# Kernel optimization log

Measured on AMD Instinct MI355X. Metric: run time of the kernel, lower is better.

## Reference

```python
import jax, jax.numpy as jnp
import numpy as np

B, L, D, K, NRBF = 2, 2048, 128, 3, 16
NUM_ATOMS = 118


def setup_inputs() -> dict:
    key = jax.random.key(0)
    ks = jax.random.split(key, 20)
    s = 0.05
    inp = {
        "coords": jax.random.normal(ks[0], (B, L, 3), dtype=jnp.float32) * 3.0,
        "Z": jax.random.randint(ks[1], (B, L), 0, NUM_ATOMS),
        # CoordEncoder params
        "atom_emb": jax.random.normal(ks[2], (NUM_ATOMS, D), dtype=jnp.float32) * s,
        "gamma": jnp.asarray(10.0, dtype=jnp.float32),
        "rbf_centers": jnp.linspace(0.0, 5.0, NRBF, dtype=jnp.float32),
        "rbf_w": jax.random.normal(ks[3], (NRBF, D), dtype=jnp.float32) * s,
        "rbf_b": jnp.zeros((D,), dtype=jnp.float32),
        "out_w": jax.random.normal(ks[4], (2 * D, D), dtype=jnp.float32) * s,
        "out_b": jnp.zeros((D,), dtype=jnp.float32),
        # MP_Layer params, stacked over K layers
        "self_w": jax.random.normal(ks[5], (K, D, D), dtype=jnp.float32) * s,
        "self_b": jnp.zeros((K, D), dtype=jnp.float32),
        "msg_w": jax.random.normal(ks[6], (K, D, D), dtype=jnp.float32) * s,
        "msg_b": jnp.zeros((K, D), dtype=jnp.float32),
        "upd_w": jax.random.normal(ks[7], (K, 2 * D, D), dtype=jnp.float32) * s,
        "upd_b": jnp.zeros((K, D), dtype=jnp.float32),
    }
    return inp


def _pairwise_dist(coords):
    # coords: [B,L,3] -> dist: [B,L,L]; safe sqrt so diagonal has zero grad
    diff = coords[:, :, None, :] - coords[:, None, :, :]
    sq = jnp.sum(diff * diff, axis=-1)
    return jnp.where(sq > 0, jnp.sqrt(jnp.where(sq > 0, sq, 1.0)), 0.0)


def reference(coords, Z, atom_emb, gamma, rbf_centers, rbf_w, rbf_b,
              out_w, out_b, self_w, self_b, msg_w, msg_b, upd_w, upd_b):
    # --- CoordEncoder ---
    h_atom = atom_emb[Z]                                   # [B,L,D]
    dist = _pairwise_dist(coords)                          # [B,L,L]
    rbf = jnp.exp(-gamma * (dist[..., None] - rbf_centers) ** 2)  # [B,L,L,R]
    rbf_local = rbf.mean(axis=2)                           # [B,L,R]
    h_geo = rbf_local @ rbf_w + rbf_b                      # [B,L,D]
    h = jnp.concatenate([h_atom, h_geo], axis=-1) @ out_w + out_b  # [B,L,D]
    # --- MP layers (mask is None; W = exp(-dist) is the same every layer) ---
    W = jnp.exp(-dist)                                     # [B,L,L]
    for k in range(K):
        msg = jnp.einsum("bij,bjd->bid", W, h @ msg_w[k] + msg_b[k])
        h = jnp.concatenate([h @ self_w[k] + self_b[k], msg], axis=-1) @ upd_w[k] + upd_b[k]
    return h
```

## Files before the change

### kernel.cpp

```cpp
#include <hip/hip_runtime.h>
#include <hip/hip_bf16.h>

typedef unsigned short u16;
typedef __bf16 bf16x8 __attribute__((ext_vector_type(8)));
typedef float f32x4 __attribute__((ext_vector_type(4)));
typedef u16 u16x4 __attribute__((ext_vector_type(4)));

#define B_ 2
#define L_ 2048
#define D_ 128
#define KLAY 3
#define NR 16
#define NATOM 118
#define DD (D_ * D_)
#define XTN (L_ * D_)

static __device__ __forceinline__ u16 f2bf(float f) {
    union { float f; unsigned u; } v; v.f = f;
    unsigned r = v.u + 0x7FFFu + ((v.u >> 16) & 1u);
    return (u16)(r >> 16);
}
static __device__ __forceinline__ bf16x8 ld_bf8(const u16* p) {
    return *(const bf16x8*)p;
}

__global__ __launch_bounds__(256) void prep_kernel(
    const float* atom_emb, const float* out_w, const float* self_w,
    const float* msg_w, const float* upd_w,
    u16* atom16, u16* outwT, u16* selfT, u16* msgT, u16* updT) {
    const int T0 = NATOM * D_;
    const int T1 = D_ * 2 * D_;
    const int T2 = KLAY * DD;
    const int T3 = KLAY * DD;
    const int T4 = KLAY * 2 * DD;
    int total = T0 + T1 + T2 + T3 + T4;
    for (int t = blockIdx.x * blockDim.x + threadIdx.x; t < total;
         t += gridDim.x * blockDim.x) {
        int u = t;
        if (u < T0) { atom16[u] = f2bf(atom_emb[u]); continue; }
        u -= T0;
        if (u < T1) {
            int n = u / (2 * D_), k = u % (2 * D_);
            outwT[u] = f2bf(out_w[k * D_ + n]);
            continue;
        }
        u -= T1;
        if (u < T2) {
            int kk = u / DD, v = u % DD;
            int n = v / D_, k = v % D_;
            selfT[u] = f2bf(self_w[kk * DD + k * D_ + n]);
            continue;
        }
        u -= T2;
        if (u < T3) {
            int kk = u / DD, v = u % DD;
            int n = v / D_, k = v % D_;
            msgT[u] = f2bf(msg_w[kk * DD + k * D_ + n]);
            continue;
        }
        u -= T3;
        {
            int kk = u / (2 * DD), v = u % (2 * DD);
            int n = v / (2 * D_), k = v % (2 * D_);
            updT[u] = f2bf(upd_w[kk * 2 * DD + k * D_ + n]);
        }
    }
}

__global__ __launch_bounds__(256) void rbf_kernel(
    const float* coords, const float* gamma_p, const float* centers,
    float* rbf_loc) {
    int w = threadIdx.x >> 6, lane = threadIdx.x & 63;
    int bi = blockIdx.x * 4 + w;
    int b = bi >> 11;
    float gamma = gamma_p[0];
    float dl = centers[1] - centers[0];
    float c4[4];
#pragma unroll
    for (int g = 0; g < 4; g++) c4[g] = centers[4 * g];
    float two_gdl = 2.f * gamma * dl;
    float cx = coords[bi * 3 + 0];
    float cy = coords[bi * 3 + 1];
    float cz = coords[bi * 3 + 2];
    const float* cb = coords + (size_t)b * L_ * 3;
    float acc[4][4];
#pragma unroll
    for (int g = 0; g < 4; g++)
#pragma unroll
        for (int m = 0; m < 4; m++) acc[g][m] = 0.f;
    for (int it = 0; it < L_ / 64; it++) {
        int j = lane + 64 * it;
        float dx = cx - cb[j * 3 + 0];
        float dy = cy - cb[j * 3 + 1];
        float dz = cz - cb[j * 3 + 2];
        float sq = dx * dx + dy * dy + dz * dz;
        float d = sq > 0.f ? sqrtf(sq) : 0.f;
#pragma unroll
        for (int g = 0; g < 4; g++) {
            float x = d - c4[g];
            float base = __expf(-gamma * x * x);
            float u = __expf(fminf(two_gdl * x, 29.f));
            float p = base;
            acc[g][0] += p;
            p *= u; acc[g][1] += p;
            p *= u; acc[g][2] += p;
            p *= u; acc[g][3] += p;
        }
    }
#pragma unroll
    for (int off = 32; off > 0; off >>= 1)
#pragma unroll
        for (int g = 0; g < 4; g++)
#pragma unroll
            for (int m = 0; m < 4; m++) acc[g][m] += __shfl_xor(acc[g][m], off);
    if (lane == 0) {
#pragma unroll
        for (int m = 0; m < 4; m++) {
            float Km = __expf(-gamma * (m * dl) * (m * dl)) * (1.0f / L_);
#pragma unroll
            for (int g = 0; g < 4; g++)
                rbf_loc[(size_t)bi * NR + 4 * g + m] = acc[g][m] * Km;
        }
    }
}

__global__ __launch_bounds__(256) void enc_sx_kernel(
    const int* Z, const float* rbf_w, const float* rbf_b, const float* out_b,
    const float* rbf_loc, const u16* atom16, const u16* outwT,
    const u16* selfT0, const u16* msgT0, const float* self_b0, const float* msg_b0,
    u16* S16, u16* XT16) {
    int gi0 = blockIdx.x * 16;
    int b = gi0 >> 11;
    int il0 = gi0 & (L_ - 1);
    int tid = threadIdx.x;
    __shared__ __align__(16) u16 hgeo[16][136];
    __shared__ __align__(16) u16 h_lds[16][136];
    for (int e = tid; e < 16 * D_; e += 256) {
        int row = e >> 7, d = e & 127;
        int gi = gi0 + row;
        float s = rbf_b[d];
#pragma unroll
        for (int r = 0; r < NR; r++)
            s += rbf_loc[(size_t)gi * NR + r] * rbf_w[r * D_ + d];
        hgeo[row][d] = f2bf(s);
    }
    __syncthreads();
    int w = tid >> 6, lane = tid & 63;
    int rowf = lane & 15, kg = lane >> 4;
    f32x4 z = {0.f, 0.f, 0.f, 0.f};
    f32x4 acc[2] = {z, z};
    int za = Z[gi0 + rowf];
    for (int ks = 0; ks < 8; ks++) {
        int k0 = ks * 32 + kg * 8;
        bf16x8 a;
        if (k0 < 128) a = ld_bf8(atom16 + za * D_ + k0);
        else a = ld_bf8(&hgeo[rowf][k0 - 128]);
#pragma unroll
        for (int q = 0; q < 2; q++) {
            int cl = (w * 2 + q) * 16 + rowf;
            bf16x8 bb = ld_bf8(outwT + cl * (2 * D_) + k0);
            acc[q] = __builtin_amdgcn_mfma_f32_16x16x32_bf16(a, bb, acc[q], 0, 0, 0);
        }
    }
#pragma unroll
    for (int q = 0; q < 2; q++) {
        int cl = (w * 2 + q) * 16 + rowf;
        float bias = out_b[cl];
#pragma unroll
        for (int r = 0; r < 4; r++) h_lds[kg * 4 + r][cl] = f2bf(acc[q][r] + bias);
    }
    __syncthreads();
    f32x4 acc3[4] = {z, z, z, z};
    for (int ks = 0; ks < 4; ks++) {
        int k0 = ks * 32 + kg * 8;
        bf16x8 a = ld_bf8(&h_lds[rowf][k0]);
#pragma unroll
        for (int q = 0; q < 4; q++) {
            int nb = w * 4 + q;
            const u16* wp = (nb < 8) ? (selfT0 + (nb * 16 + rowf) * D_ + k0)
                                     : (msgT0 + ((nb - 8) * 16 + rowf) * D_ + k0);
            acc3[q] = __builtin_amdgcn_mfma_f32_16x16x32_bf16(a, ld_bf8(wp), acc3[q], 0, 0, 0);
        }
    }
#pragma unroll
    for (int q = 0; q < 4; q++) {
        int nb = w * 4 + q;
        if (nb < 8) {
            int cl = nb * 16 + rowf;
            float bias = self_b0[cl];
#pragma unroll
            for (int r = 0; r < 4; r++)
                S16[(size_t)(gi0 + kg * 4 + r) * D_ + cl] = f2bf(acc3[q][r] + bias);
        } else {
            int cl = (nb - 8) * 16 + rowf;
            float bias = msg_b0[cl];
            u16x4 pk;
#pragma unroll
            for (int r = 0; r < 4; r++) pk[r] = f2bf(acc3[q][r] + bias);
            int jj = il0 + kg * 4;
            *(u16x4*)(XT16 + (size_t)b * XTN + (jj >> 5) * (32 * D_) + cl * 32 + (jj & 31)) = pk;
        }
    }
}

__global__ __launch_bounds__(512, 2) void mp_fused_kernel(
    const float* coords, const u16* XT_in, const u16* S_in,
    const u16* updT_k, const float* upd_b_k,
    const u16* selfTn, const u16* msgTn, const float* self_bn, const float* msg_bn,
    u16* S_out, u16* XT_out, float* out_f32, int last) {
    int gi0 = blockIdx.x * 16;
    int b = gi0 >> 11;
    int il0 = gi0 & (L_ - 1);
    int tid = threadIdx.x;
    int w = tid >> 6, lane = tid & 63;
    int rowf = lane & 15, kg = lane >> 4;

    __shared__ __align__(16) float red[4][16][128];
    __shared__ __align__(16) float cj[L_ * 3];
    u16* msg_lds = (u16*)&red[0][0][0];
    u16* h_lds = (u16*)&red[1][0][0];

    {
        const float4* src = (const float4*)(coords + (size_t)b * L_ * 3);
        float4* dst = (float4*)cj;
#pragma unroll
        for (int i = 0; i < 3; i++) dst[tid + i * 512] = src[tid + i * 512];
    }
    __syncthreads();

    float rx = cj[(il0 + rowf) * 3 + 0];
    float ry = cj[(il0 + rowf) * 3 + 1];
    float rz = cj[(il0 + rowf) * 3 + 2];

    f32x4 z = {0.f, 0.f, 0.f, 0.f};
    f32x4 acc[8] = {z, z, z, z, z, z, z, z};
    const u16* xbase = XT_in + (size_t)b * XTN + (w * 8) * (32 * D_) + rowf * 32 + kg * 8;
#pragma unroll
    for (int s = 0; s < 8; s++) {
        int j0 = w * 256 + s * 32 + kg * 8;
        const float* jc = &cj[j0 * 3];
        union { bf16x8 v; __bf16 e[8]; } wf;
#pragma unroll
        for (int e = 0; e < 8; e++) {
            float dx = rx - jc[e * 3 + 0];
            float dy = ry - jc[e * 3 + 1];
            float dz = rz - jc[e * 3 + 2];
            float sq = dx * dx + dy * dy + dz * dz;
            float d = sq > 0.f ? sqrtf(sq) : 0.f;
            wf.e[e] = (__bf16)__expf(-d);
        }
#pragma unroll
        for (int n = 0; n < 8; n++) {
            bf16x8 bb = ld_bf8(xbase + s * (32 * D_) + n * 512);
            acc[n] = __builtin_amdgcn_mfma_f32_16x16x32_bf16(wf.v, bb, acc[n], 0, 0, 0);
        }
    }
    auto stash = [&](int slot) {
#pragma unroll
        for (int n = 0; n < 8; n++)
#pragma unroll
            for (int r = 0; r < 4; r++) {
                int row = kg * 4 + r, col = n * 16 + rowf;
                red[slot][row][(col + 4 * row) & 127] = acc[n][r];
            }
    };
    auto grab = [&](int slot) {
#pragma unroll
        for (int n = 0; n < 8; n++)
#pragma unroll
            for (int r = 0; r < 4; r++) {
                int row = kg * 4 + r, col = n * 16 + rowf;
                acc[n][r] += red[slot][row][(col + 4 * row) & 127];
            }
    };
    if (w >= 4) stash(w - 4);
    __syncthreads();
    if (w < 4) grab(w);
    if (w == 2 || w == 3) stash(w);
    __syncthreads();
    if (w < 2) grab(w + 2);
    if (w == 1) stash(3);
    __syncthreads();
    if (w == 0) {
        grab(3);
#pragma unroll
        for (int n = 0; n < 8; n++)
#pragma unroll
            for (int r = 0; r < 4; r++)
                msg_lds[(kg * 4 + r) * 136 + n * 16 + rowf] = f2bf(acc[n][r]);
    }
    __syncthreads();
    f32x4 acc2 = z;
    int cl = w * 16 + rowf;
#pragma unroll
    for (int ks = 0; ks < 8; ks++) {
        int k0 = ks * 32 + kg * 8;
        bf16x8 av = (ks < 4) ? ld_bf8(S_in + (size_t)(gi0 + rowf) * D_ + k0)
                             : ld_bf8(msg_lds + rowf * 136 + (k0 - 128));
        acc2 = __builtin_amdgcn_mfma_f32_16x16x32_bf16(
            av, ld_bf8(updT_k + cl * 2 * D_ + k0), acc2, 0, 0, 0);
    }
    float bias = upd_b_k[cl];
    if (last) {
#pragma unroll
        for (int r = 0; r < 4; r++)
            out_f32[(size_t)(gi0 + kg * 4 + r) * D_ + cl] = acc2[r] + bias;
        return;
    }
#pragma unroll
    for (int r = 0; r < 4; r++)
        h_lds[(kg * 4 + r) * 136 + cl] = f2bf(acc2[r] + bias);
    __syncthreads();
    f32x4 a30 = z, a31 = z;
#pragma unroll
    for (int ks = 0; ks < 4; ks++) {
        int k0 = ks * 32 + kg * 8;
        bf16x8 av = ld_bf8(h_lds + rowf * 136 + k0);
        a30 = __builtin_amdgcn_mfma_f32_16x16x32_bf16(
            av, ld_bf8(selfTn + cl * D_ + k0), a30, 0, 0, 0);
        a31 = __builtin_amdgcn_mfma_f32_16x16x32_bf16(
            av, ld_bf8(msgTn + cl * D_ + k0), a31, 0, 0, 0);
    }
    float bs = self_bn[cl], bm = msg_bn[cl];
#pragma unroll
    for (int r = 0; r < 4; r++)
        S_out[(size_t)(gi0 + kg * 4 + r) * D_ + cl] = f2bf(a30[r] + bs);
    u16x4 pk;
#pragma unroll
    for (int r = 0; r < 4; r++) pk[r] = f2bf(a31[r] + bm);
    int jj = il0 + kg * 4;
    *(u16x4*)(XT_out + (size_t)b * XTN + (jj >> 5) * (32 * D_) + cl * 32 + (jj & 31)) = pk;
}

extern "C" void kernel_launch(void* const* d_in, const int* in_sizes, int n_in,
                              void* d_out, int out_size, void* d_ws, size_t ws_size,
                              hipStream_t stream) {
    const float* coords = (const float*)d_in[0];
    const int* Z = (const int*)d_in[1];
    const float* atom_emb = (const float*)d_in[2];
    const float* gamma = (const float*)d_in[3];
    const float* centers = (const float*)d_in[4];
    const float* rbf_w = (const float*)d_in[5];
    const float* rbf_b = (const float*)d_in[6];
    const float* out_w = (const float*)d_in[7];
    const float* out_b = (const float*)d_in[8];
    const float* self_w = (const float*)d_in[9];
    const float* self_b = (const float*)d_in[10];
    const float* msg_w = (const float*)d_in[11];
    const float* msg_b = (const float*)d_in[12];
    const float* upd_w = (const float*)d_in[13];
    const float* upd_b = (const float*)d_in[14];
    float* out = (float*)d_out;

    char* ws = (char*)d_ws;
    u16* S_a = (u16*)(ws + 0);
    u16* S_b = (u16*)(ws + 1048576);
    u16* XT_a = (u16*)(ws + 2097152);
    u16* XT_b = (u16*)(ws + 3145728);
    float* rbfl = (float*)(ws + 4194304);
    u16* atom16 = (u16*)(ws + 4456448);
    u16* outwT = (u16*)(ws + 4489216);
    u16* selfT = (u16*)(ws + 4554752);
    u16* msgT = (u16*)(ws + 4653056);
    u16* updT = (u16*)(ws + 4751360);

    prep_kernel<<<64, 256, 0, stream>>>(atom_emb, out_w, self_w, msg_w, upd_w,
                                        atom16, outwT, selfT, msgT, updT);
    rbf_kernel<<<(B_ * L_) / 4, 256, 0, stream>>>(coords, gamma, centers, rbfl);
    enc_sx_kernel<<<(B_ * L_) / 16, 256, 0, stream>>>(
        Z, rbf_w, rbf_b, out_b, rbfl, atom16, outwT,
        selfT, msgT, self_b, msg_b, S_a, XT_a);
    mp_fused_kernel<<<256, 512, 0, stream>>>(
        coords, XT_a, S_a, updT + 0 * 2 * DD, upd_b + 0 * D_,
        selfT + 1 * DD, msgT + 1 * DD, self_b + 1 * D_, msg_b + 1 * D_,
        S_b, XT_b, out, 0);
    mp_fused_kernel<<<256, 512, 0, stream>>>(
        coords, XT_b, S_b, updT + 1 * 2 * DD, upd_b + 1 * D_,
        selfT + 2 * DD, msgT + 2 * DD, self_b + 2 * D_, msg_b + 2 * D_,
        S_a, XT_a, out, 0);
    mp_fused_kernel<<<256, 512, 0, stream>>>(
        coords, XT_a, S_a, updT + 2 * 2 * DD, upd_b + 2 * D_,
        selfT, msgT, self_b, msg_b, S_b, XT_b, out, 1);
}
```

Measured before the change: 108.1 us.

## Fuse all stages into one cooperative persistent kernel with grid syncs

Replaces the six separate launches (weight prep, RBF, encoder, three MP layers) with one cooperative kernel of 256 blocks that uses grid.sync between phases. The RBF reduction and encoder now run per 16-row tile out of LDS-resident coordinates, and the self-projection S is kept in LDS instead of being round-tripped through global memory. The goal is to remove launch gaps and intermediate global traffic. In exchange it adds grid-wide barriers, and it relies on all 256 blocks of 512 threads being co-resident for the cooperative launch.

```diff
diff --git a/kernel.cpp b/kernel.cpp
--- a/kernel.cpp
+++ b/kernel.cpp
@@ -1,5 +1,8 @@
 #include <hip/hip_runtime.h>
 #include <hip/hip_bf16.h>
+#include <hip/hip_cooperative_groups.h>
+
+namespace cg = cooperative_groups;
 
 typedef unsigned short u16;
 typedef __bf16 bf16x8 __attribute__((ext_vector_type(8)));
@@ -24,312 +27,292 @@
     return *(const bf16x8*)p;
 }
 
-__global__ __launch_bounds__(256) void prep_kernel(
-    const float* atom_emb, const float* out_w, const float* self_w,
-    const float* msg_w, const float* upd_w,
+__global__ __launch_bounds__(512, 2) void uber_kernel(
+    const float* coords, const int* Z, const float* atom_emb,
+    const float* gamma_p, const float* centers, const float* rbf_w,
+    const float* rbf_b, const float* out_w, const float* out_b,
+    const float* self_w, const float* self_b, const float* msg_w,
+    const float* msg_b, const float* upd_w, const float* upd_b,
+    float* out_f32, u16* XT_a, u16* XT_b,
     u16* atom16, u16* outwT, u16* selfT, u16* msgT, u16* updT) {
-    const int T0 = NATOM * D_;
-    const int T1 = D_ * 2 * D_;
-    const int T2 = KLAY * DD;
-    const int T3 = KLAY * DD;
-    const int T4 = KLAY * 2 * DD;
-    int total = T0 + T1 + T2 + T3 + T4;
-    for (int t = blockIdx.x * blockDim.x + threadIdx.x; t < total;
-         t += gridDim.x * blockDim.x) {
-        int u = t;
-        if (u < T0) { atom16[u] = f2bf(atom_emb[u]); continue; }
-        u -= T0;
-        if (u < T1) {
-            int n = u / (2 * D_), k = u % (2 * D_);
-            outwT[u] = f2bf(out_w[k * D_ + n]);
-            continue;
-        }
-        u -= T1;
-        if (u < T2) {
-            int kk = u / DD, v = u % DD;
-            int n = v / D_, k = v % D_;
-            selfT[u] = f2bf(self_w[kk * DD + k * D_ + n]);
-            continue;
-        }
-        u -= T2;
-        if (u < T3) {
-            int kk = u / DD, v = u % DD;
-            int n = v / D_, k = v % D_;
-            msgT[u] = f2bf(msg_w[kk * DD + k * D_ + n]);
-            continue;
-        }
-        u -= T3;
-        {
-            int kk = u / (2 * DD), v = u % (2 * DD);
-            int n = v / (2 * D_), k = v % (2 * D_);
-            updT[u] = f2bf(upd_w[kk * 2 * DD + k * D_ + n]);
-        }
-    }
-}
-
-__global__ __launch_bounds__(256) void rbf_kernel(
-    const float* coords, const float* gamma_p, const float* centers,
-    float* rbf_loc) {
-    int w = threadIdx.x >> 6, lane = threadIdx.x & 63;
-    int bi = blockIdx.x * 4 + w;
-    int b = bi >> 11;
-    float gamma = gamma_p[0];
-    float dl = centers[1] - centers[0];
-    float c4[4];
-#pragma unroll
-    for (int g = 0; g < 4; g++) c4[g] = centers[4 * g];
-    float two_gdl = 2.f * gamma * dl;
-    float cx = coords[bi * 3 + 0];
-    float cy = coords[bi * 3 + 1];
-    float cz = coords[bi * 3 + 2];
-    const float* cb = coords + (size_t)b * L_ * 3;
-    float acc[4][4];
-#pragma unroll
-    for (int g = 0; g < 4; g++)
-#pragma unroll
-        for (int m = 0; m < 4; m++) acc[g][m] = 0.f;
-    for (int it = 0; it < L_ / 64; it++) {
-        int j = lane + 64 * it;
-        float dx = cx - cb[j * 3 + 0];
-        float dy = cy - cb[j * 3 + 1];
-        float dz = cz - cb[j * 3 + 2];
-        float sq = dx * dx + dy * dy + dz * dz;
-        float d = sq > 0.f ? sqrtf(sq) : 0.f;
-#pragma unroll
-        for (int g = 0; g < 4; g++) {
-            float x = d - c4[g];
-            float base = __expf(-gamma * x * x);
-            float u = __expf(fminf(two_gdl * x, 29.f));
-            float p = base;
-            acc[g][0] += p;
-            p *= u; acc[g][1] += p;
-            p *= u; acc[g][2] += p;
-            p *= u; acc[g][3] += p;
-        }
-    }
-#pragma unroll
-    for (int off = 32; off > 0; off >>= 1)
-#pragma unroll
-        for (int g = 0; g < 4; g++)
-#pragma unroll
-            for (int m = 0; m < 4; m++) acc[g][m] += __shfl_xor(acc[g][m], off);
-    if (lane == 0) {
-#pragma unroll
-        for (int m = 0; m < 4; m++) {
-            float Km = __expf(-gamma * (m * dl) * (m * dl)) * (1.0f / L_);
-#pragma unroll
-            for (int g = 0; g < 4; g++)
-                rbf_loc[(size_t)bi * NR + 4 * g + m] = acc[g][m] * Km;
-        }
-    }
-}
-
-__global__ __launch_bounds__(256) void enc_sx_kernel(
-    const int* Z, const float* rbf_w, const float* rbf_b, const float* out_b,
-    const float* rbf_loc, const u16* atom16, const u16* outwT,
-    const u16* selfT0, const u16* msgT0, const float* self_b0, const float* msg_b0,
-    u16* S16, u16* XT16) {
-    int gi0 = blockIdx.x * 16;
-    int b = gi0 >> 11;
-    int il0 = gi0 & (L_ - 1);
-    int tid = threadIdx.x;
-    __shared__ __align__(16) u16 hgeo[16][136];
-    __shared__ __align__(16) u16 h_lds[16][136];
-    for (int e = tid; e < 16 * D_; e += 256) {
-        int row = e >> 7, d = e & 127;
-        int gi = gi0 + row;
-        float s = rbf_b[d];
-#pragma unroll
-        for (int r = 0; r < NR; r++)
-            s += rbf_loc[(size_t)gi * NR + r] * rbf_w[r * D_ + d];
-        hgeo[row][d] = f2bf(s);
-    }
-    __syncthreads();
-    int w = tid >> 6, lane = tid & 63;
-    int rowf = lane & 15, kg = lane >> 4;
-    f32x4 z = {0.f, 0.f, 0.f, 0.f};
-    f32x4 acc[2] = {z, z};
-    int za = Z[gi0 + rowf];
-    for (int ks = 0; ks < 8; ks++) {
-        int k0 = ks * 32 + kg * 8;
-        bf16x8 a;
-        if (k0 < 128) a = ld_bf8(atom16 + za * D_ + k0);
-        else a = ld_bf8(&hgeo[rowf][k0 - 128]);
-#pragma unroll
-        for (int q = 0; q < 2; q++) {
-            int cl = (w * 2 + q) * 16 + rowf;
-            bf16x8 bb = ld_bf8(outwT + cl * (2 * D_) + k0);
-            acc[q] = __builtin_amdgcn_mfma_f32_16x16x32_bf16(a, bb, acc[q], 0, 0, 0);
-        }
-    }
-#pragma unroll
-    for (int q = 0; q < 2; q++) {
-        int cl = (w * 2 + q) * 16 + rowf;
-        float bias = out_b[cl];
-#pragma unroll
-        for (int r = 0; r < 4; r++) h_lds[kg * 4 + r][cl] = f2bf(acc[q][r] + bias);
-    }
-    __syncthreads();
-    f32x4 acc3[4] = {z, z, z, z};
-    for (int ks = 0; ks < 4; ks++) {
-        int k0 = ks * 32 + kg * 8;
-        bf16x8 a = ld_bf8(&h_lds[rowf][k0]);
-#pragma unroll
-        for (int q = 0; q < 4; q++) {
-            int nb = w * 4 + q;
-            const u16* wp = (nb < 8) ? (selfT0 + (nb * 16 + rowf) * D_ + k0)
-                                     : (msgT0 + ((nb - 8) * 16 + rowf) * D_ + k0);
-            acc3[q] = __builtin_amdgcn_mfma_f32_16x16x32_bf16(a, ld_bf8(wp), acc3[q], 0, 0, 0);
-        }
-    }
-#pragma unroll
-    for (int q = 0; q < 4; q++) {
-        int nb = w * 4 + q;
-        if (nb < 8) {
-            int cl = nb * 16 + rowf;
-            float bias = self_b0[cl];
-#pragma unroll
-            for (int r = 0; r < 4; r++)
-                S16[(size_t)(gi0 + kg * 4 + r) * D_ + cl] = f2bf(acc3[q][r] + bias);
-        } else {
-            int cl = (nb - 8) * 16 + rowf;
-            float bias = msg_b0[cl];
-            u16x4 pk;
-#pragma unroll
-            for (int r = 0; r < 4; r++) pk[r] = f2bf(acc3[q][r] + bias);
-            int jj = il0 + kg * 4;
-            *(u16x4*)(XT16 + (size_t)b * XTN + (jj >> 5) * (32 * D_) + cl * 32 + (jj & 31)) = pk;
-        }
-    }
-}
-
-__global__ __launch_bounds__(512, 2) void mp_fused_kernel(
-    const float* coords, const u16* XT_in, const u16* S_in,
-    const u16* updT_k, const float* upd_b_k,
-    const u16* selfTn, const u16* msgTn, const float* self_bn, const float* msg_bn,
-    u16* S_out, u16* XT_out, float* out_f32, int last) {
-    int gi0 = blockIdx.x * 16;
-    int b = gi0 >> 11;
-    int il0 = gi0 & (L_ - 1);
-    int tid = threadIdx.x;
-    int w = tid >> 6, lane = tid & 63;
-    int rowf = lane & 15, kg = lane >> 4;
-
+    cg::grid_group grid = cg::this_grid();
+    const int rt = blockIdx.x;
+    const int gi0 = rt * 16;
+    const int b = gi0 >> 11;
+    const int il0 = gi0 & (L_ - 1);
+    const int tid = threadIdx.x;
+    const int w = tid >> 6, lane = tid & 63;
+    const int rowf = lane & 15, kg = lane >> 4;
+
+    __shared__ __align__(16) float cj[L_ * 3];
     __shared__ __align__(16) float red[4][16][128];
-    __shared__ __align__(16) float cj[L_ * 3];
+    __shared__ float rbf_lds[16][NR];
+    __shared__ __align__(16) u16 s_lds[16][136];
     u16* msg_lds = (u16*)&red[0][0][0];
     u16* h_lds = (u16*)&red[1][0][0];
+    u16* hgeo = (u16*)&red[2][0][0];
+
+    for (int i = tid; i < 1536; i += 512)
+        ((float4*)cj)[i] = ((const float4*)(coords + (size_t)b * L_ * 3))[i];
 
     {
-        const float4* src = (const float4*)(coords + (size_t)b * L_ * 3);
-        float4* dst = (float4*)cj;
-#pragma unroll
-        for (int i = 0; i < 3; i++) dst[tid + i * 512] = src[tid + i * 512];
+        const int T0 = NATOM * D_;
+        const int T1 = D_ * 2 * D_;
+        const int T2 = KLAY * DD;
+        const int T3 = KLAY * DD;
+        const int T4 = KLAY * 2 * DD;
+        const int total = T0 + T1 + T2 + T3 + T4;
+        for (int t = rt * 512 + tid; t < total; t += 256 * 512) {
+            int u = t;
+            if (u < T0) { atom16[u] = f2bf(atom_emb[u]); continue; }
+            u -= T0;
+            if (u < T1) {
+                int n = u / (2 * D_), k = u % (2 * D_);
+                outwT[u] = f2bf(out_w[k * D_ + n]);
+                continue;
+            }
+            u -= T1;
+            if (u < T2) {
+                int kk = u / DD, v = u % DD;
+                int n = v / D_, k = v % D_;
+                selfT[u] = f2bf(self_w[kk * DD + k * D_ + n]);
+                continue;
+            }
+            u -= T2;
+            if (u < T3) {
+                int kk = u / DD, v = u % DD;
+                int n = v / D_, k = v % D_;
+                msgT[u] = f2bf(msg_w[kk * DD + k * D_ + n]);
+                continue;
+            }
+            u -= T3;
+            {
+                int kk = u / (2 * DD), v = u % (2 * DD);
+                int n = v / (2 * D_), k = v % (2 * D_);
+                updT[u] = f2bf(upd_w[kk * 2 * DD + k * D_ + n]);
+            }
+        }
     }
     __syncthreads();
+
+    {
+        int row = tid >> 5, s = tid & 31;
+        float gamma = gamma_p[0];
+        float dl = centers[1] - centers[0];
+        float c4[4];
+#pragma unroll
+        for (int g = 0; g < 4; g++) c4[g] = centers[4 * g];
+        float two_gdl = 2.f * gamma * dl;
+        float cx = cj[(il0 + row) * 3 + 0];
+        float cy = cj[(il0 + row) * 3 + 1];
+        float cz = cj[(il0 + row) * 3 + 2];
+        float acc[4][4];
+#pragma unroll
+        for (int g = 0; g < 4; g++)
+#pragma unroll
+            for (int m = 0; m < 4; m++) acc[g][m] = 0.f;
+        for (int it = 0; it < 64; it++) {
+            int j = s + 32 * it;
+            float dx = cx - cj[j * 3 + 0];
+            float dy = cy - cj[j * 3 + 1];
+            float dz = cz - cj[j * 3 + 2];
+            float sq = dx * dx + dy * dy + dz * dz;
+            float d = sq > 0.f ? sqrtf(sq) : 0.f;
+#pragma unroll
+            for (int g = 0; g < 4; g++) {
+                float x = d - c4[g];
+                float base = __expf(-gamma * x * x);
+                float u = __expf(fminf(two_gdl * x, 29.f));
+                float p = base;
+                acc[g][0] += p;
+                p *= u; acc[g][1] += p;
+                p *= u; acc[g][2] += p;
+                p *= u; acc[g][3] += p;
+            }
+        }
+#pragma unroll
+        for (int off = 16; off > 0; off >>= 1)
+#pragma unroll
+            for (int g = 0; g < 4; g++)
+#pragma unroll
+                for (int m = 0; m < 4; m++) acc[g][m] += __shfl_xor(acc[g][m], off);
+        if (s == 0) {
+#pragma unroll
+            for (int m = 0; m < 4; m++) {
+                float Km = __expf(-gamma * (m * dl) * (m * dl)) * (1.0f / L_);
+#pragma unroll
+                for (int g = 0; g < 4; g++)
+                    rbf_lds[row][4 * g + m] = acc[g][m] * Km;
+            }
+        }
+    }
+    grid.sync();
+
+    f32x4 z = {0.f, 0.f, 0.f, 0.f};
+
+    for (int e = tid; e < 16 * D_; e += 512) {
+        int row = e >> 7, d = e & 127;
+        float s = rbf_b[d];
+#pragma unroll
+        for (int r = 0; r < NR; r++) s += rbf_lds[row][r] * rbf_w[r * D_ + d];
+        hgeo[row * 136 + d] = f2bf(s);
+    }
+    __syncthreads();
+
+    {
+        f32x4 a1 = z;
+        int za = Z[gi0 + rowf];
+        int cl = w * 16 + rowf;
+#pragma unroll
+        for (int ks = 0; ks < 8; ks++) {
+            int k0 = ks * 32 + kg * 8;
+            bf16x8 av = (k0 < 128) ? ld_bf8(atom16 + za * D_ + k0)
+                                   : ld_bf8(hgeo + rowf * 136 + (k0 - 128));
+            a1 = __builtin_amdgcn_mfma_f32_16x16x32_bf16(
+                av, ld_bf8(outwT + cl * 2 * D_ + k0), a1, 0, 0, 0);
+        }
+        float bias = out_b[cl];
+#pragma unroll
+        for (int r = 0; r < 4; r++) h_lds[(kg * 4 + r) * 136 + cl] = f2bf(a1[r] + bias);
+    }
+    __syncthreads();
+
+    {
+        int cl = w * 16 + rowf;
+        f32x4 a30 = z, a31 = z;
+#pragma unroll
+        for (int ks = 0; ks < 4; ks++) {
+            int k0 = ks * 32 + kg * 8;
+            bf16x8 av = ld_bf8(h_lds + rowf * 136 + k0);
+            a30 = __builtin_amdgcn_mfma_f32_16x16x32_bf16(
+                av, ld_bf8(selfT + cl * D_ + k0), a30, 0, 0, 0);
+            a31 = __builtin_amdgcn_mfma_f32_16x16x32_bf16(
+                av, ld_bf8(msgT + cl * D_ + k0), a31, 0, 0, 0);
+        }
+        float bs = self_b[cl], bm = msg_b[cl];
+#pragma unroll
+        for (int r = 0; r < 4; r++) s_lds[kg * 4 + r][cl] = f2bf(a30[r] + bs);
+        u16x4 pk;
+#pragma unroll
+        for (int r = 0; r < 4; r++) pk[r] = f2bf(a31[r] + bm);
+        int jj = il0 + kg * 4;
+        *(u16x4*)(XT_a + (size_t)b * XTN + (jj >> 5) * (32 * D_) + cl * 32 + (jj & 31)) = pk;
+    }
+    grid.sync();
 
     float rx = cj[(il0 + rowf) * 3 + 0];
     float ry = cj[(il0 + rowf) * 3 + 1];
     float rz = cj[(il0 + rowf) * 3 + 2];
-
-    f32x4 z = {0.f, 0.f, 0.f, 0.f};
-    f32x4 acc[8] = {z, z, z, z, z, z, z, z};
-    const u16* xbase = XT_in + (size_t)b * XTN + (w * 8) * (32 * D_) + rowf * 32 + kg * 8;
-#pragma unroll
-    for (int s = 0; s < 8; s++) {
-        int j0 = w * 256 + s * 32 + kg * 8;
-        const float* jc = &cj[j0 * 3];
-        union { bf16x8 v; __bf16 e[8]; } wf;
-#pragma unroll
-        for (int e = 0; e < 8; e++) {
-            float dx = rx - jc[e * 3 + 0];
-            float dy = ry - jc[e * 3 + 1];
-            float dz = rz - jc[e * 3 + 2];
-            float sq = dx * dx + dy * dy + dz * dz;
-            float d = sq > 0.f ? sqrtf(sq) : 0.f;
-            wf.e[e] = (__bf16)__expf(-d);
-        }
-#pragma unroll
-        for (int n = 0; n < 8; n++) {
-            bf16x8 bb = ld_bf8(xbase + s * (32 * D_) + n * 512);
-            acc[n] = __builtin_amdgcn_mfma_f32_16x16x32_bf16(wf.v, bb, acc[n], 0, 0, 0);
-        }
-    }
-    auto stash = [&](int slot) {
-#pragma unroll
-        for (int n = 0; n < 8; n++)
-#pragma unroll
-            for (int r = 0; r < 4; r++) {
-                int row = kg * 4 + r, col = n * 16 + rowf;
-                red[slot][row][(col + 4 * row) & 127] = acc[n][r];
-            }
-    };
-    auto grab = [&](int slot) {
-#pragma unroll
-        for (int n = 0; n < 8; n++)
-#pragma unroll
-            for (int r = 0; r < 4; r++) {
-                int row = kg * 4 + r, col = n * 16 + rowf;
-                acc[n][r] += red[slot][row][(col + 4 * row) & 127];
-            }
-    };
-    if (w >= 4) stash(w - 4);
-    __syncthreads();
-    if (w < 4) grab(w);
-    if (w == 2 || w == 3) stash(w);
-    __syncthreads();
-    if (w < 2) grab(w + 2);
-    if (w == 1) stash(3);
-    __syncthreads();
-    if (w == 0) {
-        grab(3);
-#pragma unroll
-        for (int n = 0; n < 8; n++)
+    const u16* XTin = XT_a;
+    u16* XTout = XT_b;
+
+    for (int k = 0; k < KLAY; k++) {
+        f32x4 acc[8] = {z, z, z, z, z, z, z, z};
+        const u16* xbase = XTin + (size_t)b * XTN + (w * 8) * (32 * D_) + rowf * 32 + kg * 8;
+#pragma unroll
+        for (int s = 0; s < 8; s++) {
+            int j0 = w * 256 + s * 32 + kg * 8;
+            union { bf16x8 v; __bf16 e[8]; } wf;
+#pragma unroll
+            for (int e = 0; e < 8; e++) {
+                int jl = j0 + e;
+                float dx = rx - cj[jl * 3 + 0];
+                float dy = ry - cj[jl * 3 + 1];
+                float dz = rz - cj[jl * 3 + 2];
+                float sq = dx * dx + dy * dy + dz * dz;
+                float d = sq > 0.f ? sqrtf(sq) : 0.f;
+                wf.e[e] = (__bf16)__expf(-d);
+            }
+#pragma unroll
+            for (int n = 0; n < 8; n++) {
+                bf16x8 bb = ld_bf8(xbase + s * (32 * D_) + n * 512);
+                acc[n] = __builtin_amdgcn_mfma_f32_16x16x32_bf16(wf.v, bb, acc[n], 0, 0, 0);
+            }
+        }
+        auto stash = [&](int slot) {
+#pragma unroll
+            for (int n = 0; n < 8; n++)
+#pragma unroll
+                for (int r = 0; r < 4; r++) {
+                    int row = kg * 4 + r, col = n * 16 + rowf;
+                    red[slot][row][(col + 4 * row) & 127] = acc[n][r];
+                }
+        };
+        auto grab = [&](int slot) {
+#pragma unroll
+            for (int n = 0; n < 8; n++)
+#pragma unroll
+                for (int r = 0; r < 4; r++) {
+                    int row = kg * 4 + r, col = n * 16 + rowf;
+                    acc[n][r] += red[slot][row][(col + 4 * row) & 127];
+                }
+        };
+        __syncthreads();
+        if (w >= 4) stash(w - 4);
+        __syncthreads();
+        if (w < 4) grab(w);
+        if (w == 2 || w == 3) stash(w);
+        __syncthreads();
+        if (w < 2) grab(w + 2);
+        if (w == 1) stash(3);
+        __syncthreads();
+        if (w == 0) {
+            grab(3);
+#pragma unroll
+            for (int n = 0; n < 8; n++)
+#pragma unroll
+                for (int r = 0; r < 4; r++)
+                    msg_lds[(kg * 4 + r) * 136 + n * 16 + rowf] = f2bf(acc[n][r]);
+        }
+        __syncthreads();
+        const u16* updk = updT + k * 2 * DD;
+        f32x4 acc2 = z;
+        int cl = w * 16 + rowf;
+#pragma unroll
+        for (int ks = 0; ks < 8; ks++) {
+            int k0 = ks * 32 + kg * 8;
+            bf16x8 av = (ks < 4) ? ld_bf8(&s_lds[rowf][k0])
+                                 : ld_bf8(msg_lds + rowf * 136 + (k0 - 128));
+            acc2 = __builtin_amdgcn_mfma_f32_16x16x32_bf16(
+                av, ld_bf8(updk + cl * 2 * D_ + k0), acc2, 0, 0, 0);
+        }
+        float bias = upd_b[k * D_ + cl];
+        if (k == KLAY - 1) {
 #pragma unroll
             for (int r = 0; r < 4; r++)
-                msg_lds[(kg * 4 + r) * 136 + n * 16 + rowf] = f2bf(acc[n][r]);
-    }
-    __syncthreads();
-    f32x4 acc2 = z;
-    int cl = w * 16 + rowf;
-#pragma unroll
-    for (int ks = 0; ks < 8; ks++) {
-        int k0 = ks * 32 + kg * 8;
-        bf16x8 av = (ks < 4) ? ld_bf8(S_in + (size_t)(gi0 + rowf) * D_ + k0)
-                             : ld_bf8(msg_lds + rowf * 136 + (k0 - 128));
-        acc2 = __builtin_amdgcn_mfma_f32_16x16x32_bf16(
-            av, ld_bf8(updT_k + cl * 2 * D_ + k0), acc2, 0, 0, 0);
-    }
-    float bias = upd_b_k[cl];
-    if (last) {
-#pragma unroll
-        for (int r = 0; r < 4; r++)
-            out_f32[(size_t)(gi0 + kg * 4 + r) * D_ + cl] = acc2[r] + bias;
-        return;
-    }
-#pragma unroll
-    for (int r = 0; r < 4; r++)
-        h_lds[(kg * 4 + r) * 136 + cl] = f2bf(acc2[r] + bias);
-    __syncthreads();
-    f32x4 a30 = z, a31 = z;
-#pragma unroll
-    for (int ks = 0; ks < 4; ks++) {
-        int k0 = ks * 32 + kg * 8;
-        bf16x8 av = ld_bf8(h_lds + rowf * 136 + k0);
-        a30 = __builtin_amdgcn_mfma_f32_16x16x32_bf16(
-            av, ld_bf8(selfTn + cl * D_ + k0), a30, 0, 0, 0);
-        a31 = __builtin_amdgcn_mfma_f32_16x16x32_bf16(
-            av, ld_bf8(msgTn + cl * D_ + k0), a31, 0, 0, 0);
-    }
-    float bs = self_bn[cl], bm = msg_bn[cl];
-#pragma unroll
-    for (int r = 0; r < 4; r++)
-        S_out[(size_t)(gi0 + kg * 4 + r) * D_ + cl] = f2bf(a30[r] + bs);
-    u16x4 pk;
-#pragma unroll
-    for (int r = 0; r < 4; r++) pk[r] = f2bf(a31[r] + bm);
-    int jj = il0 + kg * 4;
-    *(u16x4*)(XT_out + (size_t)b * XTN + (jj >> 5) * (32 * D_) + cl * 32 + (jj & 31)) = pk;
+                out_f32[(size_t)(gi0 + kg * 4 + r) * D_ + cl] = acc2[r] + bias;
+        } else {
+#pragma unroll
+            for (int r = 0; r < 4; r++)
+                h_lds[(kg * 4 + r) * 136 + cl] = f2bf(acc2[r] + bias);
+            __syncthreads();
+            const u16* sT = selfT + (k + 1) * DD;
+            const u16* mT = msgT + (k + 1) * DD;
+            f32x4 a30 = z, a31 = z;
+#pragma unroll
+            for (int ks = 0; ks < 4; ks++) {
+                int k0 = ks * 32 + kg * 8;
+                bf16x8 av = ld_bf8(h_lds + rowf * 136 + k0);
+                a30 = __builtin_amdgcn_mfma_f32_16x16x32_bf16(
+                    av, ld_bf8(sT + cl * D_ + k0), a30, 0, 0, 0);
+                a31 = __builtin_amdgcn_mfma_f32_16x16x32_bf16(
+                    av, ld_bf8(mT + cl * D_ + k0), a31, 0, 0, 0);
+            }
+            float bs = self_b[(k + 1) * D_ + cl];
+            float bm = msg_b[(k + 1) * D_ + cl];
+#pragma unroll
+            for (int r = 0; r < 4; r++) s_lds[kg * 4 + r][cl] = f2bf(a30[r] + bs);
+            u16x4 pk;
+#pragma unroll
+            for (int r = 0; r < 4; r++) pk[r] = f2bf(a31[r] + bm);
+            int jj = il0 + kg * 4;
+            *(u16x4*)(XTout + (size_t)b * XTN + (jj >> 5) * (32 * D_) + cl * 32 + (jj & 31)) = pk;
+            grid.sync();
+            const u16* t = XTin;
+            XTin = XTout;
+            XTout = (u16*)t;
+        }
+    }
 }
 
 extern "C" void kernel_launch(void* const* d_in, const int* in_sizes, int n_in,
@@ -353,32 +336,21 @@
     float* out = (float*)d_out;
 
     char* ws = (char*)d_ws;
-    u16* S_a = (u16*)(ws + 0);
-    u16* S_b = (u16*)(ws + 1048576);
-    u16* XT_a = (u16*)(ws + 2097152);
-    u16* XT_b = (u16*)(ws + 3145728);
-    float* rbfl = (float*)(ws + 4194304);
-    u16* atom16 = (u16*)(ws + 4456448);
-    u16* outwT = (u16*)(ws + 4489216);
-    u16* selfT = (u16*)(ws + 4554752);
-    u16* msgT = (u16*)(ws + 4653056);
-    u16* updT = (u16*)(ws + 4751360);
-
-    prep_kernel<<<64, 256, 0, stream>>>(atom_emb, out_w, self_w, msg_w, upd_w,
-                                        atom16, outwT, selfT, msgT, updT);
-    rbf_kernel<<<(B_ * L_) / 4, 256, 0, stream>>>(coords, gamma, centers, rbfl);
-    enc_sx_kernel<<<(B_ * L_) / 16, 256, 0, stream>>>(
-        Z, rbf_w, rbf_b, out_b, rbfl, atom16, outwT,
-        selfT, msgT, self_b, msg_b, S_a, XT_a);
-    mp_fused_kernel<<<256, 512, 0, stream>>>(
-        coords, XT_a, S_a, updT + 0 * 2 * DD, upd_b + 0 * D_,
-        selfT + 1 * DD, msgT + 1 * DD, self_b + 1 * D_, msg_b + 1 * D_,
-        S_b, XT_b, out, 0);
-    mp_fused_kernel<<<256, 512, 0, stream>>>(
-        coords, XT_b, S_b, updT + 1 * 2 * DD, upd_b + 1 * D_,
-        selfT + 2 * DD, msgT + 2 * DD, self_b + 2 * D_, msg_b + 2 * D_,
-        S_a, XT_a, out, 0);
-    mp_fused_kernel<<<256, 512, 0, stream>>>(
-        coords, XT_a, S_a, updT + 2 * 2 * DD, upd_b + 2 * D_,
-        selfT, msgT, self_b, msg_b, S_b, XT_b, out, 1);
+    u16* XT_a = (u16*)(ws + 0);
+    u16* XT_b = (u16*)(ws + 1048576);
+    u16* atom16 = (u16*)(ws + 2097152);
+    u16* outwT = (u16*)(ws + 2129920);
+    u16* selfT = (u16*)(ws + 2195456);
+    u16* msgT = (u16*)(ws + 2293760);
+    u16* updT = (u16*)(ws + 2392064);
+
+    void* args[] = {
+        (void*)&coords, (void*)&Z, (void*)&atom_emb, (void*)&gamma,
+        (void*)&centers, (void*)&rbf_w, (void*)&rbf_b, (void*)&out_w,
+        (void*)&out_b, (void*)&self_w, (void*)&self_b, (void*)&msg_w,
+        (void*)&msg_b, (void*)&upd_w, (void*)&upd_b, (void*)&out,
+        (void*)&XT_a, (void*)&XT_b, (void*)&atom16, (void*)&outwT,
+        (void*)&selfT, (void*)&msgT, (void*)&updT};
+    hipLaunchCooperativeKernel((const void*)uber_kernel, dim3(256), dim3(512),
+                               args, 0, stream);
 }
```

New measurement: 233.2 us. 2.16x slower.
